# Performance work log

Hardware: AMD Instinct MI355X
Metric: run time of the kernel (lower is better)

## Reference

```python
import jax, jax.numpy as jnp
import numpy as np

HIDDEN = 256
OUT_T = 288


def _gru_layer(x, w_ih, w_hh, b_ih, b_hh):
    # x: (B, T, D). PyTorch GRU cell math, gates ordered [r, z, n].
    B, T, _ = x.shape
    H = w_hh.shape[1]
    xg = jnp.einsum('btd,gd->btg', x, w_ih) + b_ih  # (B, T, 3H) input-side gates

    def step(h, xg_t):
        hg = h @ w_hh.T + b_hh                      # (B, 3H)
        xr, xz, xn = jnp.split(xg_t, 3, axis=-1)
        hr, hz, hn = jnp.split(hg, 3, axis=-1)
        r = jax.nn.sigmoid(xr + hr)
        z = jax.nn.sigmoid(xz + hz)
        n = jnp.tanh(xn + r * hn)
        h_new = (1.0 - z) * n + z * h
        return h_new, h_new

    h0 = jnp.zeros((B, H), dtype=x.dtype)
    _, ys = jax.lax.scan(step, h0, jnp.swapaxes(xg, 0, 1))  # (T, B, H)
    return jnp.swapaxes(ys, 0, 1)                            # (B, T, H)


def setup_inputs() -> dict:
    key = jax.random.key(0)
    ks = jax.random.split(key, 12)
    B, T_in, D = 256, 144, 10
    H = HIDDEN
    s_in = 1.0 / np.sqrt(H)
    inp = {
        'input': jax.random.normal(ks[0], (B, T_in, D), dtype=jnp.float32),
        'w_ih_0': jax.random.uniform(ks[1], (3 * H, D), jnp.float32, -s_in, s_in),
        'w_hh_0': jax.random.uniform(ks[2], (3 * H, H), jnp.float32, -s_in, s_in),
        'b_ih_0': jax.random.uniform(ks[3], (3 * H,), jnp.float32, -s_in, s_in),
        'b_hh_0': jax.random.uniform(ks[4], (3 * H,), jnp.float32, -s_in, s_in),
        'w_ih_1': jax.random.uniform(ks[5], (3 * H, H), jnp.float32, -s_in, s_in),
        'w_hh_1': jax.random.uniform(ks[6], (3 * H, H), jnp.float32, -s_in, s_in),
        'b_ih_1': jax.random.uniform(ks[7], (3 * H,), jnp.float32, -s_in, s_in),
        'b_hh_1': jax.random.uniform(ks[8], (3 * H,), jnp.float32, -s_in, s_in),
        'w_proj': jax.random.uniform(ks[9], (1, H), jnp.float32, -s_in, s_in),
        'b_proj': jax.random.uniform(ks[10], (1,), jnp.float32, -s_in, s_in),
    }
    return inp


def reference(input, w_ih_0, w_hh_0, b_ih_0, b_hh_0,
              w_ih_1, w_hh_1, b_ih_1, b_hh_1, w_proj, b_proj):
    B = input.shape[0]
    pad = jnp.zeros((B, OUT_T, input.shape[2]), dtype=input.dtype)
    x = jnp.concatenate((input, pad), axis=1)          # (B, T_in+OUT_T, D)
    h1 = _gru_layer(x, w_ih_0, w_hh_0, b_ih_0, b_hh_0)  # (B, T, H)
    h2 = _gru_layer(h1, w_ih_1, w_hh_1, b_ih_1, b_hh_1)
    out = jnp.einsum('bth,oh->bto', h2, w_proj) + b_proj  # (B, T, 1)
    return out[:, -OUT_T:, -1:]
```

## Files before the change

### kernel.cpp

```cpp
#include <hip/hip_runtime.h>

#define THREADS 256
#define T_TOT 432
#define T_IN  144
#define T_OUT 288

#define WSTRIDE 1552
#define HA_OFF  4656
#define HB_OFF  6704
#define PRJ_OFF 35008
#define LDS_BYTES 141056


typedef float v4f __attribute__((ext_vector_type(4)));

#define FMA4(a,h,s) { a.x=fmaf((h).x,(s),a.x); a.y=fmaf((h).y,(s),a.y); \
                      a.z=fmaf((h).z,(s),a.z); a.w=fmaf((h).w,(s),a.w); }

#define VMWAIT() do { asm volatile("s_waitcnt vmcnt(0)" ::: "memory"); \
                      __builtin_amdgcn_sched_barrier(0); } while(0)

__device__ __forceinline__ float sigf(float x){ return 1.0f/(1.0f + __expf(-x)); }
__device__ __forceinline__ float tanhfast(float x){ return 1.0f - 2.0f/(__expf(2.0f*x)+1.0f); }

template<int CTRL>
__device__ __forceinline__ float4 dpp_add(float4 v){
  float4 r;
  r.x = v.x + __int_as_float(__builtin_amdgcn_update_dpp(0, __float_as_int(v.x), CTRL, 0xf, 0xf, true));
  r.y = v.y + __int_as_float(__builtin_amdgcn_update_dpp(0, __float_as_int(v.y), CTRL, 0xf, 0xf, true));
  r.z = v.z + __int_as_float(__builtin_amdgcn_update_dpp(0, __float_as_int(v.z), CTRL, 0xf, 0xf, true));
  r.w = v.w + __int_as_float(__builtin_amdgcn_update_dpp(0, __float_as_int(v.w), CTRL, 0xf, 0xf, true));
  return r;
}
__device__ __forceinline__ float4 kred4(float4 v){
  v = dpp_add<177>(v);
  v = dpp_add<78>(v);
  return v;
}

extern "C" __global__ void gru_init(float* __restrict__ ws, float* __restrict__ out,
                                    const float* __restrict__ b_proj){
  int i = blockIdx.x*THREADS + threadIdx.x;
  if (i < 262144) ws[i] = 0.0f;
  if (i < 512) ((unsigned*)(ws + 262144))[i] = 0u;
  if (i < 73728) out[i] = b_proj[0];
}

extern "C" __global__ void __launch_bounds__(THREADS, 1) gru_persist(
    const float* __restrict__ x,
    const float* __restrict__ wih0, const float* __restrict__ whh0,
    const float* __restrict__ bih0, const float* __restrict__ bhh0,
    const float* __restrict__ wih1, const float* __restrict__ whh1,
    const float* __restrict__ bih1, const float* __restrict__ bhh1,
    const float* __restrict__ wproj,
    float* __restrict__ out, float* __restrict__ ws)
{
  extern __shared__ float lds[];
  float4* WL4 = (float4*)lds;
  float4* HA4 = WL4 + HA_OFF;
  float4* HB4 = WL4 + HB_OFF;
  const float* HAf = (const float*)HA4;
  const float* HBf = (const float*)HB4;
  float* PRJ = lds + PRJ_OFF;

  const int tid = threadIdx.x;
  const int bt  = blockIdx.x & 7;
  const int g   = blockIdx.x >> 3;
  const int hi  = tid >> 5;
  const int bg  = (tid >> 2) & 7;
  const int ks  = tid & 3;
  const int bco = (bg << 2) | ks;
  const int rowg = g*8 + hi;
  const int btb  = bt << 5;

  float* h1b0 = ws;
  float* h1b1 = ws + 65536;
  float* h2b0 = ws + 131072;
  float* h2b1 = ws + 196608;
  unsigned* cntA = ((unsigned*)(ws + 262144)) + (bt << 6);
  unsigned* cntB = cntA + 32;

  {
    const float* srcs[3] = {whh0, wih1, whh1};
    #pragma unroll
    for (int m = 0; m < 3; m++){
      const float* S = srcs[m];
      for (int i = 0; i < 6; i++){
        int idx = tid + (i << 8);
        int row = idx % 24;
        int k4  = idx / 24;
        int gate = row >> 3, hh = row & 7;
        float4 v = *(const float4*)(S + (gate*256 + g*8 + hh)*256 + (k4 << 2));
        WL4[m*WSTRIDE + k4*24 + row + ((k4 >> 4) << 2)] = v;
      }
    }
  }
  float wi0[3][10];
  float bi0g[3], bh0g[3], bi1g[3], bh1g[3];
  #pragma unroll
  for (int G = 0; G < 3; G++){
    #pragma unroll
    for (int d = 0; d < 10; d++) wi0[G][d] = wih0[(G*256 + rowg)*10 + d];
    bi0g[G] = bih0[G*256 + rowg];
    bh0g[G] = bhh0[G*256 + rowg];
    bi1g[G] = bih1[G*256 + rowg];
    bh1g[G] = bhh1[G*256 + rowg];
  }
  const float wp = wproj[rowg];
  const int hIdx = (rowg << 5) + ((((bco >> 2) + ((rowg >> 6) << 1)) & 7) << 2) + (bco & 3);

  v4f hreg[8];
  auto SLOADC = [&](const float* __restrict__ hg){
    #pragma unroll
    for (int i = 0; i < 8; i++){
      int idx = tid + (i << 8);
      const float* p = hg + ((idx >> 3) << 8) + btb + ((idx & 7) << 2);
      asm volatile("global_load_dwordx4 %0, %1, off sc0 sc1"
                   : "=v"(hreg[i]) : "v"(p) : "memory");
    }
  };
  auto SWRITE = [&](float4* __restrict__ H4){
    #pragma unroll
    for (int i = 0; i < 8; i++){
      int idx = tid + (i << 8);
      int k = idx >> 3, bq = idx & 7;
      *(v4f*)&H4[(k << 3) + ((bq + ((k >> 6) << 1)) & 7)] = hreg[i];
    }
  };
  auto HSTORE = [&](float* p, float v){
    asm volatile("global_store_dword %0, %1, off sc0 sc1" :: "v"(p), "v"(v) : "memory");
  };

  auto GEMM3 = [&](const float4* __restrict__ H4, int m,
                   float4& aR, float4& aZ, float4& aN){
    const float4* Wm = WL4 + m*WSTRIDE;
    const int wo = ks*388 + hi;
    const int hb = (ks << 9) + ((bg + (ks << 1)) & 7);
    #pragma unroll 4
    for (int j = 0; j < 16; j++){
      float4 wr = Wm[wo + j*24];
      float4 wz = Wm[wo + 8 + j*24];
      float4 wn = Wm[wo + 16 + j*24];
      float4 h0 = H4[hb + (j << 5)];
      float4 h1v = H4[hb + (j << 5) + 8];
      float4 h2v = H4[hb + (j << 5) + 16];
      float4 h3v = H4[hb + (j << 5) + 24];
      FMA4(aR,h0,wr.x) FMA4(aR,h1v,wr.y) FMA4(aR,h2v,wr.z) FMA4(aR,h3v,wr.w)
      FMA4(aZ,h0,wz.x) FMA4(aZ,h1v,wz.y) FMA4(aZ,h2v,wz.z) FMA4(aZ,h3v,wz.w)
      FMA4(aN,h0,wn.x) FMA4(aN,h1v,wn.y) FMA4(aN,h2v,wn.z) FMA4(aN,h3v,wn.w)
    }
  };

  auto SEL4 = [&](float4 v){
    return ks == 0 ? v.x : (ks == 1 ? v.y : (ks == 2 ? v.z : v.w));
  };
  auto WAIT = [&](unsigned* c, unsigned tgt){
    while (__hip_atomic_fetch_add(c, 0u, __ATOMIC_RELAXED, __HIP_MEMORY_SCOPE_AGENT) < tgt)
      __builtin_amdgcn_s_sleep(4);
  };
  auto ARRIVE = [&](unsigned* c){
    __hip_atomic_fetch_add(c, 1u, __ATOMIC_RELAXED, __HIP_MEMORY_SCOPE_AGENT);
  };

  __syncthreads();
  SLOADC(h1b1);
  VMWAIT();
  SWRITE(HA4);
  __syncthreads();

  for (int t = 0; t < T_TOT; t++){
    const float* h2prev = (t & 1) ? h2b0 : h2b1;
    float* h1nxt = (t & 1) ? h1b1 : h1b0;
    float* h2nxt = (t & 1) ? h2b1 : h2b0;

    if (tid == 0) WAIT(cntB, 32u*(unsigned)t);
    __syncthreads();
    SLOADC(h2prev);

    float4 aR = {0,0,0,0}, aZ = {0,0,0,0}, aN = {0,0,0,0};
    GEMM3(HA4, 0, aR, aZ, aN);
    aR = kred4(aR); aZ = kred4(aZ); aN = kred4(aN);
    float hr = SEL4(aR) + bh0g[0];
    float hz = SEL4(aZ) + bh0g[1];
    float hn = SEL4(aN) + bh0g[2];
    float xr = bi0g[0], xz = bi0g[1], xn = bi0g[2];
    if (t < T_IN){
      const float* xp = x + (btb + bco)*(T_IN*10) + t*10;
      #pragma unroll
      for (int d = 0; d < 10; d++){
        float xv = xp[d];
        xr = fmaf(wi0[0][d], xv, xr);
        xz = fmaf(wi0[1][d], xv, xz);
        xn = fmaf(wi0[2][d], xv, xn);
      }
    }
    float r = sigf(xr + hr);
    float z = sigf(xz + hz);
    float n = tanhfast(xn + r*hn);
    float hnew1 = fmaf(z, HAf[hIdx] - n, n);
    HSTORE(h1nxt + (rowg << 8) + btb + bco, hnew1);
    VMWAIT();
    SWRITE(HB4);
    __syncthreads();
    if (tid == 0) ARRIVE(cntA);

    if (tid == 0) WAIT(cntA, 32u*(unsigned)(t + 1));
    __syncthreads();
    SLOADC(h1nxt);

    float4 bR = {0,0,0,0}, bZ = {0,0,0,0}, bN = {0,0,0,0};
    GEMM3(HB4, 2, bR, bZ, bN);
    VMWAIT();
    SWRITE(HA4);
    __syncthreads();

    float4 xR = {0,0,0,0}, xZ = {0,0,0,0}, xN = {0,0,0,0};
    GEMM3(HA4, 1, xR, xZ, xN);
    xR = kred4(xR); xZ = kred4(xZ); xN = kred4(xN);
    bR = kred4(bR); bZ = kred4(bZ); bN = kred4(bN);
    float r1 = sigf(SEL4(xR) + bi1g[0] + SEL4(bR) + bh1g[0]);
    float z1 = sigf(SEL4(xZ) + bi1g[1] + SEL4(bZ) + bh1g[1]);
    float n1 = tanhfast(SEL4(xN) + bi1g[2] + r1*(SEL4(bN) + bh1g[2]));
    float h2new = fmaf(z1, HBf[hIdx] - n1, n1);
    HSTORE(h2nxt + (rowg << 8) + btb + bco, h2new);
    if (t >= T_IN) PRJ[tid] = h2new * wp;
    VMWAIT();
    __syncthreads();
    if (tid == 0) ARRIVE(cntB);

    if (t >= T_IN && tid < 32){
      float s = 0.0f;
      #pragma unroll
      for (int hh = 0; hh < 8; hh++) s += PRJ[hh*32 + tid];
      atomicAdd(out + (btb + tid)*T_OUT + (t - T_IN), s);
    }
  }
}

extern "C" void kernel_launch(void* const* d_in, const int* in_sizes, int n_in,
                              void* d_out, int out_size, void* d_ws, size_t ws_size,
                              hipStream_t stream){
  const float* x     = (const float*)d_in[0];
  const float* wih0  = (const float*)d_in[1];
  const float* whh0  = (const float*)d_in[2];
  const float* bih0  = (const float*)d_in[3];
  const float* bhh0  = (const float*)d_in[4];
  const float* wih1  = (const float*)d_in[5];
  const float* whh1  = (const float*)d_in[6];
  const float* bih1  = (const float*)d_in[7];
  const float* bhh1  = (const float*)d_in[8];
  const float* wproj = (const float*)d_in[9];
  const float* bproj = (const float*)d_in[10];
  float* out = (float*)d_out;
  float* ws  = (float*)d_ws;

  hipLaunchKernelGGL(gru_init, dim3(1024), dim3(THREADS), 0, stream, ws, out, bproj);

  hipFuncSetAttribute(reinterpret_cast<const void*>(gru_persist),
                      hipFuncAttributeMaxDynamicSharedMemorySize, LDS_BYTES);

  void* args[] = {
    (void*)&x, (void*)&wih0, (void*)&whh0, (void*)&bih0, (void*)&bhh0,
    (void*)&wih1, (void*)&whh1, (void*)&bih1, (void*)&bhh1,
    (void*)&wproj, (void*)&out, (void*)&ws
  };
  hipLaunchCooperativeKernel(reinterpret_cast<void*>(gru_persist),
                             dim3(256), dim3(THREADS), args, LDS_BYTES, stream);
}
```

Baseline: 4.111 ms.

## Retile GRU recurrent GEMM into 4x4 register blocks and hoist layer-2 hidden GEMM before barrier

Changes the thread-to-work mapping of the per-step recurrent matmuls. Each thread now computes a 4-row by 4-column register tile over a 16-way K split, reduced with a four-stage DPP butterfly, replacing the 1-row by 4-column tile with a 4-way K split. This raises FMA work per LDS load and changes the LDS swizzles for weights and hidden state to match. It also moves the layer-2 hidden-to-hidden GEMM ahead of the cross-block wait, so it overlaps with other blocks finishing layer 1. The larger accumulator arrays increase register pressure, and the wider reduction adds DPP and select work.

New measurement: 4.275 ms. 4.0% more time.

```diff
diff --git a/kernel.cpp b/kernel.cpp
--- a/kernel.cpp
+++ b/kernel.cpp
@@ -5,14 +5,12 @@
 #define T_IN  144
 #define T_OUT 288
 
-#define WSTRIDE 1552
+#define WS4     1552
 #define HA_OFF  4656
 #define HB_OFF  6704
-#define PRJ_OFF 35008
+#define PRJ_OFFf 35008
 #define LDS_BYTES 141056
 
-
-typedef float v4f __attribute__((ext_vector_type(4)));
 
 #define FMA4(a,h,s) { a.x=fmaf((h).x,(s),a.x); a.y=fmaf((h).y,(s),a.y); \
                       a.z=fmaf((h).z,(s),a.z); a.w=fmaf((h).w,(s),a.w); }
@@ -32,9 +30,11 @@
   r.w = v.w + __int_as_float(__builtin_amdgcn_update_dpp(0, __float_as_int(v.w), CTRL, 0xf, 0xf, true));
   return r;
 }
-__device__ __forceinline__ float4 kred4(float4 v){
+__device__ __forceinline__ float4 kred16(float4 v){
   v = dpp_add<177>(v);
   v = dpp_add<78>(v);
+  v = dpp_add<0x141>(v);
+  v = dpp_add<0x140>(v);
   return v;
 }
 
@@ -45,6 +45,8 @@
   if (i < 512) ((unsigned*)(ws + 262144))[i] = 0u;
   if (i < 73728) out[i] = b_proj[0];
 }
+
+typedef float v4f __attribute__((ext_vector_type(4)));
 
 extern "C" __global__ void __launch_bounds__(THREADS, 1) gru_persist(
     const float* __restrict__ x,
@@ -61,16 +63,19 @@
   float4* HB4 = WL4 + HB_OFF;
   const float* HAf = (const float*)HA4;
   const float* HBf = (const float*)HB4;
-  float* PRJ = lds + PRJ_OFF;
+  float* PRJ = lds + PRJ_OFFf;
 
   const int tid = threadIdx.x;
   const int bt  = blockIdx.x & 7;
   const int g   = blockIdx.x >> 3;
-  const int hi  = tid >> 5;
-  const int bg  = (tid >> 2) & 7;
-  const int ks  = tid & 3;
-  const int bco = (bg << 2) | ks;
-  const int rowg = g*8 + hi;
+  const int kg   = tid & 15;
+  const int qglo = (tid >> 4) & 3;
+  const int wv   = tid >> 6;
+  const int rh   = wv >> 1;
+  const int cq   = ((wv & 1) << 2) | qglo;
+  const int hrow = (rh << 2) | (kg >> 2);
+  const int col  = (cq << 2) | (kg & 3);
+  const int rowg = g*8 + hrow;
   const int btb  = bt << 5;
 
   float* h1b0 = ws;
@@ -91,7 +96,7 @@
         int k4  = idx / 24;
         int gate = row >> 3, hh = row & 7;
         float4 v = *(const float4*)(S + (gate*256 + g*8 + hh)*256 + (k4 << 2));
-        WL4[m*WSTRIDE + k4*24 + row + ((k4 >> 4) << 2)] = v;
+        WL4[m*WS4 + k4*24 + row + (k4 >> 2)] = v;
       }
     }
   }
@@ -107,7 +112,7 @@
     bh1g[G] = bhh1[G*256 + rowg];
   }
   const float wp = wproj[rowg];
-  const int hIdx = (rowg << 5) + ((((bco >> 2) + ((rowg >> 6) << 1)) & 7) << 2) + (bco & 3);
+  const int hIdx = (rowg << 5) + ((((col >> 2) + (rowg >> 4)) & 7) << 2) + (col & 3);
 
   v4f hreg[8];
   auto SLOADC = [&](const float* __restrict__ hg){
@@ -123,37 +128,59 @@
     #pragma unroll
     for (int i = 0; i < 8; i++){
       int idx = tid + (i << 8);
-      int k = idx >> 3, bq = idx & 7;
-      *(v4f*)&H4[(k << 3) + ((bq + ((k >> 6) << 1)) & 7)] = hreg[i];
+      int k = idx >> 3, q = idx & 7;
+      *(v4f*)&H4[(k << 3) + ((q + (k >> 4)) & 7)] = hreg[i];
     }
   };
   auto HSTORE = [&](float* p, float v){
     asm volatile("global_store_dword %0, %1, off sc0 sc1" :: "v"(p), "v"(v) : "memory");
   };
 
-  auto GEMM3 = [&](const float4* __restrict__ H4, int m,
-                   float4& aR, float4& aZ, float4& aN){
-    const float4* Wm = WL4 + m*WSTRIDE;
-    const int wo = ks*388 + hi;
-    const int hb = (ks << 9) + ((bg + (ks << 1)) & 7);
-    #pragma unroll 4
-    for (int j = 0; j < 16; j++){
-      float4 wr = Wm[wo + j*24];
-      float4 wz = Wm[wo + 8 + j*24];
-      float4 wn = Wm[wo + 16 + j*24];
-      float4 h0 = H4[hb + (j << 5)];
-      float4 h1v = H4[hb + (j << 5) + 8];
-      float4 h2v = H4[hb + (j << 5) + 16];
-      float4 h3v = H4[hb + (j << 5) + 24];
-      FMA4(aR,h0,wr.x) FMA4(aR,h1v,wr.y) FMA4(aR,h2v,wr.z) FMA4(aR,h3v,wr.w)
-      FMA4(aZ,h0,wz.x) FMA4(aZ,h1v,wz.y) FMA4(aZ,h2v,wz.z) FMA4(aZ,h3v,wz.w)
-      FMA4(aN,h0,wn.x) FMA4(aN,h1v,wn.y) FMA4(aN,h2v,wn.z) FMA4(aN,h3v,wn.w)
-    }
-  };
-
-  auto SEL4 = [&](float4 v){
-    return ks == 0 ? v.x : (ks == 1 ? v.y : (ks == 2 ? v.z : v.w));
-  };
+  auto GEMM3 = [&](const float4* __restrict__ H4, int m, float4 (&acc)[3][4]){
+    const int wb = m*WS4;
+    #pragma unroll
+    for (int j = 0; j < 4; j++){
+      const int k4 = (kg << 2) + j;
+      const int wr = wb + k4*24 + (k4 >> 2);
+      float4 wf[3][4];
+      #pragma unroll
+      for (int gte = 0; gte < 3; gte++)
+        #pragma unroll
+        for (int ri = 0; ri < 4; ri++)
+          wf[gte][ri] = WL4[wr + (gte << 3) + (rh << 2) + ri];
+      #pragma unroll
+      for (int dk = 0; dk < 4; dk++){
+        const int kidx = (k4 << 2) + dk;
+        float4 hv = H4[(kidx << 3) + ((cq + kg) & 7)];
+        #pragma unroll
+        for (int gte = 0; gte < 3; gte++)
+          #pragma unroll
+          for (int ri = 0; ri < 4; ri++){
+            float wsv = dk == 0 ? wf[gte][ri].x : dk == 1 ? wf[gte][ri].y :
+                        dk == 2 ? wf[gte][ri].z : wf[gte][ri].w;
+            FMA4(acc[gte][ri], hv, wsv);
+          }
+      }
+    }
+  };
+  auto REDEX = [&](float4 (&acc)[3][4], float* g3){
+    #pragma unroll
+    for (int gte = 0; gte < 3; gte++)
+      #pragma unroll
+      for (int ri = 0; ri < 4; ri++)
+        acc[gte][ri] = kred16(acc[gte][ri]);
+    const int r = kg >> 2, c = kg & 3;
+    #pragma unroll
+    for (int gte = 0; gte < 3; gte++){
+      float4 f0 = (r & 2) ? acc[gte][2] : acc[gte][0];
+      float4 f1 = (r & 2) ? acc[gte][3] : acc[gte][1];
+      float4 f  = (r & 1) ? f1 : f0;
+      float e0 = (c & 2) ? f.z : f.x;
+      float e1 = (c & 2) ? f.w : f.y;
+      g3[gte] = (c & 1) ? e1 : e0;
+    }
+  };
+
   auto WAIT = [&](unsigned* c, unsigned tgt){
     while (__hip_atomic_fetch_add(c, 0u, __ATOMIC_RELAXED, __HIP_MEMORY_SCOPE_AGENT) < tgt)
       __builtin_amdgcn_s_sleep(4);
@@ -177,53 +204,52 @@
     __syncthreads();
     SLOADC(h2prev);
 
-    float4 aR = {0,0,0,0}, aZ = {0,0,0,0}, aN = {0,0,0,0};
-    GEMM3(HA4, 0, aR, aZ, aN);
-    aR = kred4(aR); aZ = kred4(aZ); aN = kred4(aN);
-    float hr = SEL4(aR) + bh0g[0];
-    float hz = SEL4(aZ) + bh0g[1];
-    float hn = SEL4(aN) + bh0g[2];
+    float4 acc0[3][4] = {};
+    GEMM3(HA4, 0, acc0);
+    float g0[3];
+    REDEX(acc0, g0);
     float xr = bi0g[0], xz = bi0g[1], xn = bi0g[2];
     if (t < T_IN){
-      const float* xp = x + (btb + bco)*(T_IN*10) + t*10;
+      const float* xp = x + (btb + col)*(T_IN*10) + t*10;
       #pragma unroll
       for (int d = 0; d < 10; d++){
-        float xv = xp[d];
-        xr = fmaf(wi0[0][d], xv, xr);
-        xz = fmaf(wi0[1][d], xv, xz);
-        xn = fmaf(wi0[2][d], xv, xn);
+        float xvv = xp[d];
+        xr = fmaf(wi0[0][d], xvv, xr);
+        xz = fmaf(wi0[1][d], xvv, xz);
+        xn = fmaf(wi0[2][d], xvv, xn);
       }
     }
-    float r = sigf(xr + hr);
-    float z = sigf(xz + hz);
-    float n = tanhfast(xn + r*hn);
+    float r = sigf(xr + g0[0] + bh0g[0]);
+    float z = sigf(xz + g0[1] + bh0g[1]);
+    float n = tanhfast(xn + r*(g0[2] + bh0g[2]));
     float hnew1 = fmaf(z, HAf[hIdx] - n, n);
-    HSTORE(h1nxt + (rowg << 8) + btb + bco, hnew1);
+    HSTORE(h1nxt + (rowg << 8) + btb + col, hnew1);
     VMWAIT();
     SWRITE(HB4);
     __syncthreads();
     if (tid == 0) ARRIVE(cntA);
 
+    float4 acc2[3][4] = {};
+    GEMM3(HB4, 2, acc2);
+    float g2[3];
+    REDEX(acc2, g2);
     if (tid == 0) WAIT(cntA, 32u*(unsigned)(t + 1));
     __syncthreads();
     SLOADC(h1nxt);
-
-    float4 bR = {0,0,0,0}, bZ = {0,0,0,0}, bN = {0,0,0,0};
-    GEMM3(HB4, 2, bR, bZ, bN);
     VMWAIT();
     SWRITE(HA4);
     __syncthreads();
 
-    float4 xR = {0,0,0,0}, xZ = {0,0,0,0}, xN = {0,0,0,0};
-    GEMM3(HA4, 1, xR, xZ, xN);
-    xR = kred4(xR); xZ = kred4(xZ); xN = kred4(xN);
-    bR = kred4(bR); bZ = kred4(bZ); bN = kred4(bN);
-    float r1 = sigf(SEL4(xR) + bi1g[0] + SEL4(bR) + bh1g[0]);
-    float z1 = sigf(SEL4(xZ) + bi1g[1] + SEL4(bZ) + bh1g[1]);
-    float n1 = tanhfast(SEL4(xN) + bi1g[2] + r1*(SEL4(bN) + bh1g[2]));
+    float4 acc1[3][4] = {};
+    GEMM3(HA4, 1, acc1);
+    float g1[3];
+    REDEX(acc1, g1);
+    float r1 = sigf(g1[0] + bi1g[0] + g2[0] + bh1g[0]);
+    float z1 = sigf(g1[1] + bi1g[1] + g2[1] + bh1g[1]);
+    float n1 = tanhfast(g1[2] + bi1g[2] + r1*(g2[2] + bh1g[2]));
     float h2new = fmaf(z1, HBf[hIdx] - n1, n1);
-    HSTORE(h2nxt + (rowg << 8) + btb + bco, h2new);
-    if (t >= T_IN) PRJ[tid] = h2new * wp;
+    HSTORE(h2nxt + (rowg << 8) + btb + col, h2new);
+    if (t >= T_IN) PRJ[(hrow << 5) + col] = h2new * wp;
     VMWAIT();
     __syncthreads();
     if (tid == 0) ARRIVE(cntB);
```
